# Kernel tuning notes

Hardware: AMD Instinct MI355X
Metric: run time of the kernel (lower is better)

## Reference

```python
import jax, jax.numpy as jnp
import numpy as np

B, N, DIM, H, DH, M = 2, 2048, 1024, 16, 64, 512
INNER = H * DH  # 1024
KV = M + 1 + N  # xl mem + null kv + sequence = 2561


def rotate_half(x):
    x1, x2 = jnp.split(x, 2, axis=-1)
    return jnp.concatenate([-x2, x1], axis=-1)


def apply_rotary_pos_emb(pos, t):
    return t * jnp.cos(pos) + rotate_half(t) * jnp.sin(pos)


def setup_inputs() -> dict:
    key = jax.random.key(0)
    ks = jax.random.split(key, 8)
    return {
        "x": jax.random.normal(ks[0], (B, N, DIM), jnp.float32),
        "rotary_q": jax.random.uniform(ks[1], (N, DH), jnp.float32) * 6.28,
        "rotary_k": jax.random.uniform(ks[2], (KV, DH), jnp.float32) * 6.28,
        "xl_memories": jax.random.normal(ks[3], (2, B, H, M, DH), jnp.float32) * 0.02,
        "Wq": jax.random.normal(ks[4], (DIM, INNER), jnp.float32) * 0.02,
        "Wkv": jax.random.normal(ks[5], (DIM, 2 * INNER), jnp.float32) * 0.02,
        "Wout": jax.random.normal(ks[6], (INNER, INNER), jnp.float32) * 0.02,
        "null_kv": jax.random.normal(ks[7], (2, H, DH), jnp.float32),
    }


def reference(x, rotary_q, rotary_k, xl_memories, Wq, Wkv, Wout, null_kv):
    # QKV projections (no bias, matching keras Dense(use_bias=False))
    q = (x @ Wq).reshape(B, N, H, DH).transpose(0, 2, 1, 3)  # b h n d
    k, v = jnp.split(x @ Wkv, 2, axis=-1)
    k = k.reshape(B, N, H, DH).transpose(0, 2, 1, 3)
    v = v.reshape(B, N, H, DH).transpose(0, 2, 1, 3)

    # prepend learned null key/value (1 token)
    nk = jnp.broadcast_to(null_kv[0][None, :, None, :], (B, H, 1, DH))
    nv = jnp.broadcast_to(null_kv[1][None, :, None, :], (B, H, 1, DH))
    k = jnp.concatenate([nk, k], axis=2)
    v = jnp.concatenate([nv, v], axis=2)

    next_xl_memories = jnp.stack([k, v])  # [2, b, h, 1+n, d]

    # prepend XL memories along key axis
    k = jnp.concatenate([xl_memories[0], k], axis=2)  # b h kv d
    v = jnp.concatenate([xl_memories[1], v], axis=2)

    # inline rotary embedding on q and (full) k
    q = apply_rotary_pos_emb(rotary_q, q)
    k = apply_rotary_pos_emb(rotary_k, k)

    # causal attention with bottom-right aligned mask (mem/null tokens visible)
    scale = DH ** -0.5
    sim = jnp.einsum('bhid,bhjd->bhij', q, k) * scale  # b h n kv
    i = jnp.arange(N)[:, None]
    j = jnp.arange(KV)[None, :]
    causal_ok = j <= (i + (KV - N))
    sim = jnp.where(causal_ok, sim, jnp.finfo(sim.dtype).min)
    attn = jax.nn.softmax(sim, axis=-1)
    out = jnp.einsum('bhij,bhjd->bhid', attn, v)  # b h n d

    out = out.transpose(0, 2, 1, 3).reshape(B, N, INNER)
    return out @ Wout, next_xl_memories
```

## Files before the change

### kernel.cpp

```cpp
#include <hip/hip_runtime.h>
#include <hip/hip_bf16.h>


typedef short v8s __attribute__((ext_vector_type(8)));
typedef float v4f __attribute__((ext_vector_type(4)));

__device__ __forceinline__ float bf2f(unsigned short x) {
  return __uint_as_float(((unsigned)x) << 16);
}
__device__ __forceinline__ unsigned short f2bf(float f) {
  unsigned u = __float_as_uint(f);
  u += 0x7FFFu + ((u >> 16) & 1u);
  return (unsigned short)(u >> 16);
}

#if __has_builtin(__builtin_amdgcn_exp2f)
#define EXP2(x) __builtin_amdgcn_exp2f(x)
#else
#define EXP2(x) exp2f(x)
#endif

__device__ __forceinline__ void gld_lds16(const void* g, void* l) {
  __builtin_amdgcn_global_load_lds(
      (const __attribute__((address_space(1))) unsigned int*)g,
      (__attribute__((address_space(3))) unsigned int*)l, 16, 0, 0);
}

__device__ __forceinline__ unsigned pk_bf16(float lo, float hi) {
  union { __hip_bfloat162 h; unsigned u; } cv;
  cv.h = __float22bfloat162_rn(make_float2(lo, hi));
  return cv.u;
}

__global__ __launch_bounds__(256) void cvt_bf16(
    const float* __restrict__ S, unsigned short* __restrict__ D, int n4)
{
  const int i = blockIdx.x * 256 + threadIdx.x;
  if (i < n4) {
    const float4 v = ((const float4*)S)[i];
    ushort4 o;
    o.x = f2bf(v.x); o.y = f2bf(v.y); o.z = f2bf(v.z); o.w = f2bf(v.w);
    ((ushort4*)D)[i] = o;
  }
}

template <typename CT>
__global__ __launch_bounds__(256, 2) void gemm_bf16(
    const unsigned short* __restrict__ A,
    const unsigned short* __restrict__ WT,
    CT* __restrict__ C,
    int K, int ldc)
{
  __shared__ unsigned short As[128 * 64];
  __shared__ unsigned short Bs[128 * 64];
  const int tid  = threadIdx.x;
  const int wave = tid >> 6, lane = tid & 63;
  const int l15  = lane & 15, quad = lane >> 4;
  const int wm   = wave >> 1, wn = wave & 1;
  const int row0 = blockIdx.x * 128, col0 = blockIdx.y * 128;
  const int lrow = lane >> 3;
  const int gsw  = (lane & 7) ^ lrow;

  v4f acc[4][4];
  const v4f vzero = {0.f, 0.f, 0.f, 0.f};
#pragma unroll
  for (int i = 0; i < 4; ++i)
#pragma unroll
    for (int j = 0; j < 4; ++j) acc[i][j] = vzero;

  for (int k0 = 0; k0 < K; k0 += 64) {
    __syncthreads();
#pragma unroll
    for (int ro = 0; ro < 4; ++ro) {
      const int chunk = wave * 4 + ro;
      const int arow  = chunk * 8 + lrow;
      gld_lds16(A  + (size_t)(row0 + arow) * K + k0 + gsw * 8, As + chunk * 512);
      gld_lds16(WT + (size_t)(col0 + arow) * K + k0 + gsw * 8, Bs + chunk * 512);
    }
    __syncthreads();

    v8s af[4][2], bf[4][2];
#pragma unroll
    for (int tm = 0; tm < 4; ++tm) {
      const int r = wm * 64 + tm * 16 + l15;
#pragma unroll
      for (int kk = 0; kk < 2; ++kk) {
        const int slot = (kk * 4 + quad) ^ (r & 7);
        af[tm][kk] = *(const v8s*)(As + r * 64 + slot * 8);
      }
    }
#pragma unroll
    for (int tn = 0; tn < 4; ++tn) {
      const int r = wn * 64 + tn * 16 + l15;
#pragma unroll
      for (int kk = 0; kk < 2; ++kk) {
        const int slot = (kk * 4 + quad) ^ (r & 7);
        bf[tn][kk] = *(const v8s*)(Bs + r * 64 + slot * 8);
      }
    }
#pragma unroll
    for (int kk = 0; kk < 2; ++kk)
#pragma unroll
      for (int tm = 0; tm < 4; ++tm)
#pragma unroll
        for (int tn = 0; tn < 4; ++tn)
          acc[tm][tn] = __builtin_amdgcn_mfma_f32_16x16x32_bf16(
              af[tm][kk], bf[tn][kk], acc[tm][tn], 0, 0, 0);
  }

#pragma unroll
  for (int tm = 0; tm < 4; ++tm)
#pragma unroll
    for (int tn = 0; tn < 4; ++tn)
#pragma unroll
      for (int r = 0; r < 4; ++r) {
        const int row = row0 + wm * 64 + tm * 16 + quad * 4 + r;
        const int col = col0 + wn * 64 + tn * 16 + l15;
        if constexpr (sizeof(CT) == 2)
          C[(size_t)row * ldc + col] = (CT)f2bf(acc[tm][tn][r]);
        else
          C[(size_t)row * ldc + col] = (CT)acc[tm][tn][r];
      }
}

__global__ __launch_bounds__(256) void transpose_wt(
    const float* __restrict__ S0,
    const float* __restrict__ S1,
    int c0, int c1, int K,
    unsigned short* __restrict__ D)
{
  __shared__ float T[64][65];
  const int k0 = blockIdx.x * 64, n0 = blockIdx.y * 64;
  const int tid = threadIdx.x;
#pragma unroll
  for (int ro = 0; ro < 4; ++ro) {
    const int idx = ro * 256 + tid;
    const int kr = idx >> 4, ch = idx & 15;
    const int n = n0 + ch * 4;
    float4 val;
    if (n < c0) val = *(const float4*)(S0 + (size_t)(k0 + kr) * c0 + n);
    else        val = *(const float4*)(S1 + (size_t)(k0 + kr) * c1 + (n - c0));
    T[kr][ch * 4 + 0] = val.x; T[kr][ch * 4 + 1] = val.y;
    T[kr][ch * 4 + 2] = val.z; T[kr][ch * 4 + 3] = val.w;
  }
  __syncthreads();
#pragma unroll
  for (int ro = 0; ro < 2; ++ro) {
    const int idx = ro * 256 + tid;
    const int nl = idx >> 3, ch = idx & 7;
    __align__(16) unsigned short tmp[8];
#pragma unroll
    for (int e = 0; e < 8; ++e) tmp[e] = f2bf(T[ch * 8 + e][nl]);
    *(uint4*)(D + (size_t)(n0 + nl) * K + k0 + ch * 8) = *(const uint4*)tmp;
  }
}

__global__ __launch_bounds__(256) void assemble(
    const unsigned short* __restrict__ QKV,
    const float* __restrict__ rq,
    const float* __restrict__ rk,
    const float* __restrict__ xlm,
    const float* __restrict__ nkv,
    unsigned short* __restrict__ Qrot,
    unsigned short* __restrict__ Kf,
    unsigned short* __restrict__ Vn,
    float* __restrict__ nxl)
{
  const int gw = blockIdx.x * 4 + (threadIdx.x >> 6);
  const int d  = threadIdx.x & 63;
  const int RK = 32 * 2561;
  const int RQ = 32 * 2048;
  if (gw < RK) {
    const int bh = gw / 2561;
    const int j  = gw - bh * 2561;
    const int b  = bh >> 4, h = bh & 15;
    float kx, vx;
    if (j < 512) {
      const size_t i0 = (((size_t)(b * 16 + h)) * 512 + j) * 64 + d;
      kx = xlm[i0];
      vx = xlm[1048576 + i0];
    } else if (j == 512) {
      kx = nkv[h * 64 + d];
      vx = nkv[1024 + h * 64 + d];
    } else {
      const size_t rowb = ((size_t)(b * 2048 + (j - 513))) * 3072;
      kx = bf2f(QKV[rowb + 1024 + h * 64 + d]);
      vx = bf2f(QKV[rowb + 2048 + h * 64 + d]);
    }
    Vn[(((size_t)bh) * 2561 + j) * 64 + d] = f2bf(vx);
    if (j >= 512) {
      const size_t o0 = (((size_t)(b * 16 + h)) * 2049 + (j - 512)) * 64 + d;
      nxl[o0] = kx;
      nxl[4196352 + o0] = vx;
    }
    const float ang = rk[j * 64 + d];
    const float cs = __cosf(ang), sn = __sinf(ang);
    const float part = __shfl_xor(kx, 32);
    const float kr = kx * cs + (d < 32 ? -part : part) * sn;
    Kf[(((size_t)bh) * 2624 + j) * 64 + d] = f2bf(kr);
  } else if (gw < RK + RQ) {
    const int g2 = gw - RK;
    const int bh = g2 >> 11, n = g2 & 2047;
    const int b  = bh >> 4, h = bh & 15;
    const float qx = bf2f(QKV[((size_t)(b * 2048 + n)) * 3072 + h * 64 + d]);
    const float ang = rq[n * 64 + d];
    const float cs = __cosf(ang), sn = __sinf(ang);
    const float part = __shfl_xor(qx, 32);
    const float qr = qx * cs + (d < 32 ? -part : part) * sn;
    Qrot[(((size_t)bh) * 2048 + n) * 64 + d] = f2bf(qr * 0.18033688f);
  } else {
    const int g3 = gw - RK - RQ;
    const int bh = g3 / 63;
    const int jj = 2561 + (g3 - bh * 63);
    Kf[(((size_t)bh) * 2624 + jj) * 64 + d] = 0;
  }
}

__global__ __launch_bounds__(256) void transpose_v(
    const unsigned short* __restrict__ Vn,
    unsigned short* __restrict__ VTp)
{
  __shared__ unsigned short T[64][72];
  const int j0 = blockIdx.x * 64;
  const int bh = blockIdx.y;
  const int tid = threadIdx.x;
#pragma unroll
  for (int ro = 0; ro < 2; ++ro) {
    const int idx = ro * 256 + tid;
    const int jr = idx >> 3, ch = idx & 7;
    uint4 val = make_uint4(0, 0, 0, 0);
    if (j0 + jr < 2561)
      val = *(const uint4*)(Vn + (((size_t)bh) * 2561 + j0 + jr) * 64 + ch * 8);
    *(uint4*)(&T[jr][ch * 8]) = val;
  }
  __syncthreads();
#pragma unroll
  for (int ro = 0; ro < 2; ++ro) {
    const int idx = ro * 256 + tid;
    const int dl = idx >> 3, ch = idx & 7;
    __align__(16) unsigned short tmp[8];
#pragma unroll
    for (int e = 0; e < 8; ++e) {
      const int kappa = ch * 8 + e;
      const int sig = (kappa & 32) + ((e & 4) << 2) + ((ch & 3) << 2) + (e & 3);
      tmp[e] = T[sig][dl];
    }
    *(uint4*)(VTp + (((size_t)bh) * 64 + dl) * 2624 + j0 + ch * 8) = *(const uint4*)tmp;
  }
}

__global__ __launch_bounds__(256, 4) void attn_fa(
    const unsigned short* __restrict__ Qr,
    const unsigned short* __restrict__ Kf,
    const unsigned short* __restrict__ VTp,
    unsigned short* __restrict__ Ao)
{
  const int bh = blockIdx.y;
  const int qb = 31 - (int)((blockIdx.x + blockIdx.y) & 31);
  const int b = bh >> 4, h = bh & 15;
  __shared__ unsigned short Ks[2][64 * 72];
  __shared__ unsigned short Vs[2][64 * 72];
  const int tid = threadIdx.x;
  const int wave = tid >> 6, lane = tid & 63;
  const int l15 = lane & 15, quad = lane >> 4;
  const v4f vzero = {0.f, 0.f, 0.f, 0.f};

  v8s qf[2];
  {
    const unsigned short* Qg =
        Qr + (((size_t)bh) * 2048 + qb * 64 + wave * 16 + l15) * 64;
    qf[0] = *(const v8s*)(Qg + quad * 8);
    qf[1] = *(const v8s*)(Qg + 32 + quad * 8);
  }
  const int qbase = qb * 64 + wave * 16 + l15 + 513;

  v4f O[4], Ol;
#pragma unroll
  for (int dt = 0; dt < 4; ++dt) O[dt] = vzero;
  Ol = vzero;
  const short one_bf = (short)0x3F80;
  const v8s ones = {one_bf, one_bf, one_bf, one_bf,
                    one_bf, one_bf, one_bf, one_bf};

  const unsigned short* Kg0 = Kf + (size_t)bh * 2624 * 64;
  const unsigned short* Vg0 = VTp + (size_t)bh * 64 * 2624;
  const int ntiles = (qb + 10 <= 41) ? (qb + 10) : 41;
  const int tfast  = qb + 7;

  const int srow = tid >> 3, sch = tid & 7;
  const int srow1 = srow + 32;
  uint4 ka, kb, va, vb;

#define PREFETCH(t)                                                          \
  {                                                                          \
    const int j0p = (t) * 64;                                                \
    ka = *(const uint4*)(Kg0 + (size_t)(j0p + srow) * 64 + sch * 8);         \
    va = *(const uint4*)(Vg0 + (size_t)srow * 2624 + j0p + sch * 8);         \
    kb = *(const uint4*)(Kg0 + (size_t)(j0p + srow1) * 64 + sch * 8);        \
    vb = *(const uint4*)(Vg0 + (size_t)srow1 * 2624 + j0p + sch * 8);        \
  }
#define STAGE(bi)                                                            \
  {                                                                          \
    *(uint4*)(Ks[bi] + srow * 72 + sch * 8) = ka;                            \
    *(uint4*)(Vs[bi] + srow * 72 + sch * 8) = va;                            \
    *(uint4*)(Ks[bi] + srow1 * 72 + sch * 8) = kb;                           \
    *(uint4*)(Vs[bi] + srow1 * 72 + sch * 8) = vb;                           \
  }

  auto compute_tile = [&](const unsigned short* Ksb, const unsigned short* Vsb,
                          int j0, bool masked) {
    v4f s[4];
#pragma unroll
    for (int jt = 0; jt < 4; ++jt) {
      const v8s kfr0 = *(const v8s*)(Ksb + (jt * 16 + l15) * 72 + quad * 8);
      const v8s kfr1 = *(const v8s*)(Ksb + (jt * 16 + l15) * 72 + 32 + quad * 8);
      v4f c = vzero;
      c = __builtin_amdgcn_mfma_f32_16x16x32_bf16(kfr0, qf[0], c, 0, 0, 0);
      c = __builtin_amdgcn_mfma_f32_16x16x32_bf16(kfr1, qf[1], c, 0, 0, 0);
      s[jt] = c;
    }

    if (masked) {
#pragma unroll
      for (int jt = 0; jt < 4; ++jt) {
        const int jrow = j0 + jt * 16 + quad * 4;
#pragma unroll
        for (int r = 0; r < 4; ++r)
          s[jt][r] = (jrow + r <= qbase) ? s[jt][r] : -1e30f;
      }
    }

    union { unsigned u[4]; v8s s8; } pk0, pk1;
    pk0.u[0] = pk_bf16(EXP2(s[0][0]), EXP2(s[0][1]));
    pk0.u[1] = pk_bf16(EXP2(s[0][2]), EXP2(s[0][3]));
    pk0.u[2] = pk_bf16(EXP2(s[1][0]), EXP2(s[1][1]));
    pk0.u[3] = pk_bf16(EXP2(s[1][2]), EXP2(s[1][3]));
    pk1.u[0] = pk_bf16(EXP2(s[2][0]), EXP2(s[2][1]));
    pk1.u[1] = pk_bf16(EXP2(s[2][2]), EXP2(s[2][3]));
    pk1.u[2] = pk_bf16(EXP2(s[3][0]), EXP2(s[3][1]));
    pk1.u[3] = pk_bf16(EXP2(s[3][2]), EXP2(s[3][3]));

#pragma unroll
    for (int dt = 0; dt < 4; ++dt) {
      const v8s vf0 = *(const v8s*)(Vsb + (dt * 16 + l15) * 72 + quad * 8);
      const v8s vf1 = *(const v8s*)(Vsb + (dt * 16 + l15) * 72 + 32 + quad * 8);
      v4f c = O[dt];
      c = __builtin_amdgcn_mfma_f32_16x16x32_bf16(pk0.s8, vf0, c, 0, 0, 0);
      c = __builtin_amdgcn_mfma_f32_16x16x32_bf16(pk1.s8, vf1, c, 0, 0, 0);
      O[dt] = c;
    }
    Ol = __builtin_amdgcn_mfma_f32_16x16x32_bf16(pk0.s8, ones, Ol, 0, 0, 0);
    Ol = __builtin_amdgcn_mfma_f32_16x16x32_bf16(pk1.s8, ones, Ol, 0, 0, 0);
  };

  PREFETCH(0);
  STAGE(0);
  PREFETCH(1);
  __syncthreads();
  for (int t = 0; t < ntiles; ++t) {
    if (t + 1 < ntiles) {
      STAGE((t + 1) & 1);
      if (t + 2 < ntiles) PREFETCH(t + 2);
    }
    compute_tile(Ks[t & 1], Vs[t & 1], t * 64, t > tfast);
    __syncthreads();
  }
#undef PREFETCH
#undef STAGE

#pragma unroll
  for (int r = 0; r < 4; ++r) {
    const float linv = 1.0f / Ol[r];
    const int n = qb * 64 + wave * 16 + quad * 4 + r;
    const size_t rowbase = ((size_t)b * 2048 + n) * 1024 + h * 64;
#pragma unroll
    for (int dt = 0; dt < 4; ++dt)
      Ao[rowbase + dt * 16 + l15] = f2bf(O[dt][r] * linv);
  }
}

extern "C" void kernel_launch(void* const* d_in, const int* in_sizes, int n_in,
                              void* d_out, int out_size, void* d_ws, size_t ws_size,
                              hipStream_t stream)
{
  const float* x    = (const float*)d_in[0];
  const float* rq   = (const float*)d_in[1];
  const float* rk   = (const float*)d_in[2];
  const float* xlm  = (const float*)d_in[3];
  const float* Wq   = (const float*)d_in[4];
  const float* Wkv  = (const float*)d_in[5];
  const float* Wout = (const float*)d_in[6];
  const float* nkv  = (const float*)d_in[7];
  float* out = (float*)d_out;
  float* nxl = out + 4194304;
  char* ws = (char*)d_ws;
  unsigned short* QKV   = (unsigned short*)(ws + 0);
  unsigned short* xbf   = (unsigned short*)(ws + 25165824);
  unsigned short* Ao    = (unsigned short*)(ws + 25165824);
  unsigned short* WqkvT = (unsigned short*)(ws + 33554432);
  unsigned short* WoutT = (unsigned short*)(ws + 39845888);
  unsigned short* Qrot  = (unsigned short*)(ws + 41943040);
  unsigned short* Kf    = (unsigned short*)(ws + 50331648);
  unsigned short* Vn    = (unsigned short*)(ws + 61079552);
  unsigned short* VTp   = (unsigned short*)(ws + 71569408);

  cvt_bf16<<<4096, 256, 0, stream>>>(x, xbf, 1048576);
  transpose_wt<<<dim3(16, 48), 256, 0, stream>>>(Wq, Wkv, 1024, 2048, 1024, WqkvT);
  transpose_wt<<<dim3(16, 16), 256, 0, stream>>>(Wout, Wout, 1024, 1024, 1024, WoutT);
  gemm_bf16<unsigned short><<<dim3(32, 24), 256, 0, stream>>>(xbf, WqkvT, QKV, 1024, 3072);
  assemble<<<37376, 256, 0, stream>>>(QKV, rq, rk, xlm, nkv, Qrot, Kf, Vn, nxl);
  transpose_v<<<dim3(41, 32), 256, 0, stream>>>(Vn, VTp);
  attn_fa<<<dim3(32, 32), 256, 0, stream>>>(Qrot, Kf, VTp, Ao);
  gemm_bf16<float><<<dim3(32, 8), 256, 0, stream>>>(Ao, WoutT, out, 1024, 1024);
}
```

Before: 229.5 us.

## Switch attention to 32x32 MFMA with direct global K/V fragment loads

Rewrites the attention kernel so each 64-thread wave handles 32 query rows using 32x32x16 bf16 MFMA instead of 16x16x32 tiles. The block drops to 128 threads and no longer stages K/V through double-buffered LDS; each lane loads its MFMA fragments straight from global memory. The V transpose permutation and the block-to-work mapping change to match. This removes the LDS staging and barrier cost and raises MFMA work per instruction, but relies on cache hits for the repeated K/V reads and leaves global load latency exposed with no explicit prefetch.

```diff
diff --git a/kernel.cpp b/kernel.cpp
--- a/kernel.cpp
+++ b/kernel.cpp
@@ -4,6 +4,7 @@
 
 typedef short v8s __attribute__((ext_vector_type(8)));
 typedef float v4f __attribute__((ext_vector_type(4)));
+typedef float v16f __attribute__((ext_vector_type(16)));
 
 __device__ __forceinline__ float bf2f(unsigned short x) {
   return __uint_as_float(((unsigned)x) << 16);
@@ -241,141 +242,124 @@
     __align__(16) unsigned short tmp[8];
 #pragma unroll
     for (int e = 0; e < 8; ++e) {
-      const int kappa = ch * 8 + e;
-      const int sig = (kappa & 32) + ((e & 4) << 2) + ((ch & 3) << 2) + (e & 3);
+      const int sig = (e & 3) + ((ch & 3) << 2) + ((e & 4) << 2) + ((ch & 4) << 3);
       tmp[e] = T[sig][dl];
     }
     *(uint4*)(VTp + (((size_t)bh) * 64 + dl) * 2624 + j0 + ch * 8) = *(const uint4*)tmp;
   }
 }
 
-__global__ __launch_bounds__(256, 4) void attn_fa(
+__global__ __launch_bounds__(128, 2) void attn_fa(
     const unsigned short* __restrict__ Qr,
     const unsigned short* __restrict__ Kf,
     const unsigned short* __restrict__ VTp,
     unsigned short* __restrict__ Ao)
 {
-  const int bh = blockIdx.y;
-  const int qb = 31 - (int)((blockIdx.x + blockIdx.y) & 31);
+  const int bh = blockIdx.x;
+  const int qb = 31 - (int)((blockIdx.x * 9 + blockIdx.y) & 31);
   const int b = bh >> 4, h = bh & 15;
-  __shared__ unsigned short Ks[2][64 * 72];
-  __shared__ unsigned short Vs[2][64 * 72];
   const int tid = threadIdx.x;
-  const int wave = tid >> 6, lane = tid & 63;
-  const int l15 = lane & 15, quad = lane >> 4;
-  const v4f vzero = {0.f, 0.f, 0.f, 0.f};
-
-  v8s qf[2];
+  const int w = tid >> 6;
+  const int lane = tid & 63;
+  const int l31 = lane & 31, hf = lane >> 5;
+
+  v8s qf[4];
   {
     const unsigned short* Qg =
-        Qr + (((size_t)bh) * 2048 + qb * 64 + wave * 16 + l15) * 64;
-    qf[0] = *(const v8s*)(Qg + quad * 8);
-    qf[1] = *(const v8s*)(Qg + 32 + quad * 8);
-  }
-  const int qbase = qb * 64 + wave * 16 + l15 + 513;
-
-  v4f O[4], Ol;
-#pragma unroll
-  for (int dt = 0; dt < 4; ++dt) O[dt] = vzero;
-  Ol = vzero;
+        Qr + (((size_t)bh) * 2048 + qb * 64 + w * 32 + l31) * 64 + hf * 8;
+#pragma unroll
+    for (int kb = 0; kb < 4; ++kb) qf[kb] = *(const v8s*)(Qg + kb * 16);
+  }
+  const int qbase = qb * 64 + w * 32 + l31 + 513;
+
+  v16f O0 = {0,0,0,0,0,0,0,0,0,0,0,0,0,0,0,0};
+  v16f O1 = {0,0,0,0,0,0,0,0,0,0,0,0,0,0,0,0};
+  v16f Olv = {0,0,0,0,0,0,0,0,0,0,0,0,0,0,0,0};
   const short one_bf = (short)0x3F80;
   const v8s ones = {one_bf, one_bf, one_bf, one_bf,
                     one_bf, one_bf, one_bf, one_bf};
 
-  const unsigned short* Kg0 = Kf + (size_t)bh * 2624 * 64;
-  const unsigned short* Vg0 = VTp + (size_t)bh * 64 * 2624;
-  const int ntiles = (qb + 10 <= 41) ? (qb + 10) : 41;
+  const unsigned short* Kg =
+      Kf + ((size_t)bh * 2624 + l31) * 64 + hf * 8;
+  const unsigned short* V0 =
+      VTp + ((size_t)bh * 64 + l31) * 2624 + hf * 8;
+  const unsigned short* V1 = V0 + (size_t)32 * 2624;
+
+  const int ntiles = qb + 10;
   const int tfast  = qb + 7;
 
-  const int srow = tid >> 3, sch = tid & 7;
-  const int srow1 = srow + 32;
-  uint4 ka, kb, va, vb;
-
-#define PREFETCH(t)                                                          \
-  {                                                                          \
-    const int j0p = (t) * 64;                                                \
-    ka = *(const uint4*)(Kg0 + (size_t)(j0p + srow) * 64 + sch * 8);         \
-    va = *(const uint4*)(Vg0 + (size_t)srow * 2624 + j0p + sch * 8);         \
-    kb = *(const uint4*)(Kg0 + (size_t)(j0p + srow1) * 64 + sch * 8);        \
-    vb = *(const uint4*)(Vg0 + (size_t)srow1 * 2624 + j0p + sch * 8);        \
-  }
-#define STAGE(bi)                                                            \
-  {                                                                          \
-    *(uint4*)(Ks[bi] + srow * 72 + sch * 8) = ka;                            \
-    *(uint4*)(Vs[bi] + srow * 72 + sch * 8) = va;                            \
-    *(uint4*)(Ks[bi] + srow1 * 72 + sch * 8) = kb;                           \
-    *(uint4*)(Vs[bi] + srow1 * 72 + sch * 8) = vb;                           \
-  }
-
-  auto compute_tile = [&](const unsigned short* Ksb, const unsigned short* Vsb,
-                          int j0, bool masked) {
-    v4f s[4];
-#pragma unroll
-    for (int jt = 0; jt < 4; ++jt) {
-      const v8s kfr0 = *(const v8s*)(Ksb + (jt * 16 + l15) * 72 + quad * 8);
-      const v8s kfr1 = *(const v8s*)(Ksb + (jt * 16 + l15) * 72 + 32 + quad * 8);
-      v4f c = vzero;
-      c = __builtin_amdgcn_mfma_f32_16x16x32_bf16(kfr0, qf[0], c, 0, 0, 0);
-      c = __builtin_amdgcn_mfma_f32_16x16x32_bf16(kfr1, qf[1], c, 0, 0, 0);
-      s[jt] = c;
-    }
-
-    if (masked) {
-#pragma unroll
-      for (int jt = 0; jt < 4; ++jt) {
-        const int jrow = j0 + jt * 16 + quad * 4;
-#pragma unroll
-        for (int r = 0; r < 4; ++r)
-          s[jt][r] = (jrow + r <= qbase) ? s[jt][r] : -1e30f;
-      }
-    }
-
-    union { unsigned u[4]; v8s s8; } pk0, pk1;
-    pk0.u[0] = pk_bf16(EXP2(s[0][0]), EXP2(s[0][1]));
-    pk0.u[1] = pk_bf16(EXP2(s[0][2]), EXP2(s[0][3]));
-    pk0.u[2] = pk_bf16(EXP2(s[1][0]), EXP2(s[1][1]));
-    pk0.u[3] = pk_bf16(EXP2(s[1][2]), EXP2(s[1][3]));
-    pk1.u[0] = pk_bf16(EXP2(s[2][0]), EXP2(s[2][1]));
-    pk1.u[1] = pk_bf16(EXP2(s[2][2]), EXP2(s[2][3]));
-    pk1.u[2] = pk_bf16(EXP2(s[3][0]), EXP2(s[3][1]));
-    pk1.u[3] = pk_bf16(EXP2(s[3][2]), EXP2(s[3][3]));
-
-#pragma unroll
-    for (int dt = 0; dt < 4; ++dt) {
-      const v8s vf0 = *(const v8s*)(Vsb + (dt * 16 + l15) * 72 + quad * 8);
-      const v8s vf1 = *(const v8s*)(Vsb + (dt * 16 + l15) * 72 + 32 + quad * 8);
-      v4f c = O[dt];
-      c = __builtin_amdgcn_mfma_f32_16x16x32_bf16(pk0.s8, vf0, c, 0, 0, 0);
-      c = __builtin_amdgcn_mfma_f32_16x16x32_bf16(pk1.s8, vf1, c, 0, 0, 0);
-      O[dt] = c;
-    }
-    Ol = __builtin_amdgcn_mfma_f32_16x16x32_bf16(pk0.s8, ones, Ol, 0, 0, 0);
-    Ol = __builtin_amdgcn_mfma_f32_16x16x32_bf16(pk1.s8, ones, Ol, 0, 0, 0);
-  };
-
-  PREFETCH(0);
-  STAGE(0);
-  PREFETCH(1);
-  __syncthreads();
   for (int t = 0; t < ntiles; ++t) {
-    if (t + 1 < ntiles) {
-      STAGE((t + 1) & 1);
-      if (t + 2 < ntiles) PREFETCH(t + 2);
-    }
-    compute_tile(Ks[t & 1], Vs[t & 1], t * 64, t > tfast);
-    __syncthreads();
-  }
-#undef PREFETCH
-#undef STAGE
-
-#pragma unroll
-  for (int r = 0; r < 4; ++r) {
-    const float linv = 1.0f / Ol[r];
-    const int n = qb * 64 + wave * 16 + quad * 4 + r;
+    const int j64 = t * 64;
+
+    v8s kf0[4], kf1[4];
+    {
+      const unsigned short* Kl = Kg + (size_t)j64 * 64;
+#pragma unroll
+      for (int kb = 0; kb < 4; ++kb) {
+        kf0[kb] = *(const v8s*)(Kl + kb * 16);
+        kf1[kb] = *(const v8s*)(Kl + 2048 + kb * 16);
+      }
+    }
+
+    v16f s0 = {0,0,0,0,0,0,0,0,0,0,0,0,0,0,0,0};
+    v16f s1 = {0,0,0,0,0,0,0,0,0,0,0,0,0,0,0,0};
+#pragma unroll
+    for (int kb = 0; kb < 4; ++kb) {
+      s0 = __builtin_amdgcn_mfma_f32_32x32x16_bf16(kf0[kb], qf[kb], s0, 0, 0, 0);
+      s1 = __builtin_amdgcn_mfma_f32_32x32x16_bf16(kf1[kb], qf[kb], s1, 0, 0, 0);
+    }
+
+    if (t > tfast) {
+#pragma unroll
+      for (int reg = 0; reg < 16; ++reg) {
+        const int krow = (reg & 3) + 8 * (reg >> 2) + 4 * hf;
+        s0[reg] = (j64 + krow <= qbase) ? s0[reg] : -1e30f;
+        s1[reg] = (j64 + 32 + krow <= qbase) ? s1[reg] : -1e30f;
+      }
+    }
+
+    union PK { unsigned u[4]; v8s s8; };
+    PK pa00, pa01, pa10, pa11;
+    pa00.u[0] = pk_bf16(EXP2(s0[0]),  EXP2(s0[1]));
+    pa00.u[1] = pk_bf16(EXP2(s0[2]),  EXP2(s0[3]));
+    pa00.u[2] = pk_bf16(EXP2(s0[8]),  EXP2(s0[9]));
+    pa00.u[3] = pk_bf16(EXP2(s0[10]), EXP2(s0[11]));
+    pa01.u[0] = pk_bf16(EXP2(s0[4]),  EXP2(s0[5]));
+    pa01.u[1] = pk_bf16(EXP2(s0[6]),  EXP2(s0[7]));
+    pa01.u[2] = pk_bf16(EXP2(s0[12]), EXP2(s0[13]));
+    pa01.u[3] = pk_bf16(EXP2(s0[14]), EXP2(s0[15]));
+    pa10.u[0] = pk_bf16(EXP2(s1[0]),  EXP2(s1[1]));
+    pa10.u[1] = pk_bf16(EXP2(s1[2]),  EXP2(s1[3]));
+    pa10.u[2] = pk_bf16(EXP2(s1[8]),  EXP2(s1[9]));
+    pa10.u[3] = pk_bf16(EXP2(s1[10]), EXP2(s1[11]));
+    pa11.u[0] = pk_bf16(EXP2(s1[4]),  EXP2(s1[5]));
+    pa11.u[1] = pk_bf16(EXP2(s1[6]),  EXP2(s1[7]));
+    pa11.u[2] = pk_bf16(EXP2(s1[12]), EXP2(s1[13]));
+    pa11.u[3] = pk_bf16(EXP2(s1[14]), EXP2(s1[15]));
+
+#define PV_STEP(pa_, kvoff)                                                   \
+    {                                                                         \
+      const v8s vf0 = *(const v8s*)(V0 + j64 + (kvoff));                      \
+      const v8s vf1 = *(const v8s*)(V1 + j64 + (kvoff));                      \
+      O0  = __builtin_amdgcn_mfma_f32_32x32x16_bf16(pa_.s8, vf0,  O0,  0,0,0);\
+      O1  = __builtin_amdgcn_mfma_f32_32x32x16_bf16(pa_.s8, vf1,  O1,  0,0,0);\
+      Olv = __builtin_amdgcn_mfma_f32_32x32x16_bf16(pa_.s8, ones, Olv, 0,0,0);\
+    }
+    PV_STEP(pa00, 0);
+    PV_STEP(pa01, 16);
+    PV_STEP(pa10, 32);
+    PV_STEP(pa11, 48);
+#undef PV_STEP
+  }
+
+#pragma unroll
+  for (int reg = 0; reg < 16; ++reg) {
+    const int qloc = (reg & 3) + 8 * (reg >> 2) + 4 * hf;
+    const float linv = 1.0f / Olv[reg];
+    const int n = qb * 64 + w * 32 + qloc;
     const size_t rowbase = ((size_t)b * 2048 + n) * 1024 + h * 64;
-#pragma unroll
-    for (int dt = 0; dt < 4; ++dt)
-      Ao[rowbase + dt * 16 + l15] = f2bf(O[dt][r] * linv);
+    Ao[rowbase + l31]      = f2bf(O0[reg] * linv);
+    Ao[rowbase + 32 + l31] = f2bf(O1[reg] * linv);
   }
 }
 
@@ -410,6 +394,6 @@
   gemm_bf16<unsigned short><<<dim3(32, 24), 256, 0, stream>>>(xbf, WqkvT, QKV, 1024, 3072);
   assemble<<<37376, 256, 0, stream>>>(QKV, rq, rk, xlm, nkv, Qrot, Kf, Vn, nxl);
   transpose_v<<<dim3(41, 32), 256, 0, stream>>>(Vn, VTp);
-  attn_fa<<<dim3(32, 32), 256, 0, stream>>>(Qrot, Kf, VTp, Ao);
+  attn_fa<<<dim3(32, 32), 128, 0, stream>>>(Qrot, Kf, VTp, Ao);
   gemm_bf16<float><<<dim3(32, 8), 256, 0, stream>>>(Ao, WoutT, out, 1024, 1024);
 }
```

Measured after the change: 298.5 us. +30.0%, slower.

## Give each attention wave two 16-row query tiles and halve block size

Applied to the files above, without the earlier changes.

The flash-attention kernel now runs 2 waves per block instead of 4, with each wave handling 32 query rows as two 16-row MFMA tiles. Each K/V fragment read from LDS is reused across both query tiles, which halves LDS fragment traffic per FLOP. Each thread also stages four rows of K and V instead of two. The cost is higher register pressure (doubled O accumulators and score tiles) and fewer threads per block to hide latency. Launch bounds also change to (128, 2).

```diff
diff --git a/kernel.cpp b/kernel.cpp
--- a/kernel.cpp
+++ b/kernel.cpp
@@ -249,7 +249,7 @@
   }
 }
 
-__global__ __launch_bounds__(256, 4) void attn_fa(
+__global__ __launch_bounds__(128, 2) void attn_fa(
     const unsigned short* __restrict__ Qr,
     const unsigned short* __restrict__ Kf,
     const unsigned short* __restrict__ VTp,
@@ -261,23 +261,28 @@
   __shared__ unsigned short Ks[2][64 * 72];
   __shared__ unsigned short Vs[2][64 * 72];
   const int tid = threadIdx.x;
-  const int wave = tid >> 6, lane = tid & 63;
+  const int wave = tid >> 6;
+  const int lane = tid & 63;
   const int l15 = lane & 15, quad = lane >> 4;
   const v4f vzero = {0.f, 0.f, 0.f, 0.f};
 
-  v8s qf[2];
-  {
+  v8s qf[2][2];
+#pragma unroll
+  for (int mt = 0; mt < 2; ++mt) {
     const unsigned short* Qg =
-        Qr + (((size_t)bh) * 2048 + qb * 64 + wave * 16 + l15) * 64;
-    qf[0] = *(const v8s*)(Qg + quad * 8);
-    qf[1] = *(const v8s*)(Qg + 32 + quad * 8);
-  }
-  const int qbase = qb * 64 + wave * 16 + l15 + 513;
-
-  v4f O[4], Ol;
-#pragma unroll
-  for (int dt = 0; dt < 4; ++dt) O[dt] = vzero;
-  Ol = vzero;
+        Qr + (((size_t)bh) * 2048 + qb * 64 + wave * 32 + mt * 16 + l15) * 64;
+    qf[mt][0] = *(const v8s*)(Qg + quad * 8);
+    qf[mt][1] = *(const v8s*)(Qg + 32 + quad * 8);
+  }
+  const int qb0 = qb * 64 + wave * 32 + l15 + 513;
+
+  v4f O[2][4], Ol[2];
+#pragma unroll
+  for (int mt = 0; mt < 2; ++mt) {
+#pragma unroll
+    for (int dt = 0; dt < 4; ++dt) O[mt][dt] = vzero;
+    Ol[mt] = vzero;
+  }
   const short one_bf = (short)0x3F80;
   const v8s ones = {one_bf, one_bf, one_bf, one_bf,
                     one_bf, one_bf, one_bf, one_bf};
@@ -288,69 +293,89 @@
   const int tfast  = qb + 7;
 
   const int srow = tid >> 3, sch = tid & 7;
-  const int srow1 = srow + 32;
-  uint4 ka, kb, va, vb;
+  uint4 kk[4], vv[4];
 
 #define PREFETCH(t)                                                          \
   {                                                                          \
     const int j0p = (t) * 64;                                                \
-    ka = *(const uint4*)(Kg0 + (size_t)(j0p + srow) * 64 + sch * 8);         \
-    va = *(const uint4*)(Vg0 + (size_t)srow * 2624 + j0p + sch * 8);         \
-    kb = *(const uint4*)(Kg0 + (size_t)(j0p + srow1) * 64 + sch * 8);        \
-    vb = *(const uint4*)(Vg0 + (size_t)srow1 * 2624 + j0p + sch * 8);        \
+    _Pragma("unroll")                                                        \
+    for (int i = 0; i < 4; ++i) {                                            \
+      kk[i] = *(const uint4*)(Kg0 + (size_t)(j0p + srow + 16 * i) * 64 +     \
+                              sch * 8);                                      \
+      vv[i] = *(const uint4*)(Vg0 + (size_t)(srow + 16 * i) * 2624 + j0p +   \
+                              sch * 8);                                      \
+    }                                                                        \
   }
 #define STAGE(bi)                                                            \
   {                                                                          \
-    *(uint4*)(Ks[bi] + srow * 72 + sch * 8) = ka;                            \
-    *(uint4*)(Vs[bi] + srow * 72 + sch * 8) = va;                            \
-    *(uint4*)(Ks[bi] + srow1 * 72 + sch * 8) = kb;                           \
-    *(uint4*)(Vs[bi] + srow1 * 72 + sch * 8) = vb;                           \
+    _Pragma("unroll")                                                        \
+    for (int i = 0; i < 4; ++i) {                                            \
+      *(uint4*)(Ks[bi] + (srow + 16 * i) * 72 + sch * 8) = kk[i];            \
+      *(uint4*)(Vs[bi] + (srow + 16 * i) * 72 + sch * 8) = vv[i];            \
+    }                                                                        \
   }
 
   auto compute_tile = [&](const unsigned short* Ksb, const unsigned short* Vsb,
                           int j0, bool masked) {
-    v4f s[4];
+    v4f s[2][4];
 #pragma unroll
     for (int jt = 0; jt < 4; ++jt) {
       const v8s kfr0 = *(const v8s*)(Ksb + (jt * 16 + l15) * 72 + quad * 8);
       const v8s kfr1 = *(const v8s*)(Ksb + (jt * 16 + l15) * 72 + 32 + quad * 8);
-      v4f c = vzero;
-      c = __builtin_amdgcn_mfma_f32_16x16x32_bf16(kfr0, qf[0], c, 0, 0, 0);
-      c = __builtin_amdgcn_mfma_f32_16x16x32_bf16(kfr1, qf[1], c, 0, 0, 0);
-      s[jt] = c;
+#pragma unroll
+      for (int mt = 0; mt < 2; ++mt) {
+        v4f c = vzero;
+        c = __builtin_amdgcn_mfma_f32_16x16x32_bf16(kfr0, qf[mt][0], c, 0, 0, 0);
+        c = __builtin_amdgcn_mfma_f32_16x16x32_bf16(kfr1, qf[mt][1], c, 0, 0, 0);
+        s[mt][jt] = c;
+      }
     }
 
     if (masked) {
 #pragma unroll
-      for (int jt = 0; jt < 4; ++jt) {
-        const int jrow = j0 + jt * 16 + quad * 4;
-#pragma unroll
-        for (int r = 0; r < 4; ++r)
-          s[jt][r] = (jrow + r <= qbase) ? s[jt][r] : -1e30f;
-      }
-    }
-
-    union { unsigned u[4]; v8s s8; } pk0, pk1;
-    pk0.u[0] = pk_bf16(EXP2(s[0][0]), EXP2(s[0][1]));
-    pk0.u[1] = pk_bf16(EXP2(s[0][2]), EXP2(s[0][3]));
-    pk0.u[2] = pk_bf16(EXP2(s[1][0]), EXP2(s[1][1]));
-    pk0.u[3] = pk_bf16(EXP2(s[1][2]), EXP2(s[1][3]));
-    pk1.u[0] = pk_bf16(EXP2(s[2][0]), EXP2(s[2][1]));
-    pk1.u[1] = pk_bf16(EXP2(s[2][2]), EXP2(s[2][3]));
-    pk1.u[2] = pk_bf16(EXP2(s[3][0]), EXP2(s[3][1]));
-    pk1.u[3] = pk_bf16(EXP2(s[3][2]), EXP2(s[3][3]));
+      for (int mt = 0; mt < 2; ++mt) {
+        const int qbase = qb0 + mt * 16;
+#pragma unroll
+        for (int jt = 0; jt < 4; ++jt) {
+          const int jrow = j0 + jt * 16 + quad * 4;
+#pragma unroll
+          for (int r = 0; r < 4; ++r)
+            s[mt][jt][r] = (jrow + r <= qbase) ? s[mt][jt][r] : -1e30f;
+        }
+      }
+    }
+
+    union PK { unsigned u[4]; v8s s8; };
+    PK pk0[2], pk1[2];
+#pragma unroll
+    for (int mt = 0; mt < 2; ++mt) {
+      pk0[mt].u[0] = pk_bf16(EXP2(s[mt][0][0]), EXP2(s[mt][0][1]));
+      pk0[mt].u[1] = pk_bf16(EXP2(s[mt][0][2]), EXP2(s[mt][0][3]));
+      pk0[mt].u[2] = pk_bf16(EXP2(s[mt][1][0]), EXP2(s[mt][1][1]));
+      pk0[mt].u[3] = pk_bf16(EXP2(s[mt][1][2]), EXP2(s[mt][1][3]));
+      pk1[mt].u[0] = pk_bf16(EXP2(s[mt][2][0]), EXP2(s[mt][2][1]));
+      pk1[mt].u[1] = pk_bf16(EXP2(s[mt][2][2]), EXP2(s[mt][2][3]));
+      pk1[mt].u[2] = pk_bf16(EXP2(s[mt][3][0]), EXP2(s[mt][3][1]));
+      pk1[mt].u[3] = pk_bf16(EXP2(s[mt][3][2]), EXP2(s[mt][3][3]));
+    }
 
 #pragma unroll
     for (int dt = 0; dt < 4; ++dt) {
       const v8s vf0 = *(const v8s*)(Vsb + (dt * 16 + l15) * 72 + quad * 8);
       const v8s vf1 = *(const v8s*)(Vsb + (dt * 16 + l15) * 72 + 32 + quad * 8);
-      v4f c = O[dt];
-      c = __builtin_amdgcn_mfma_f32_16x16x32_bf16(pk0.s8, vf0, c, 0, 0, 0);
-      c = __builtin_amdgcn_mfma_f32_16x16x32_bf16(pk1.s8, vf1, c, 0, 0, 0);
-      O[dt] = c;
-    }
-    Ol = __builtin_amdgcn_mfma_f32_16x16x32_bf16(pk0.s8, ones, Ol, 0, 0, 0);
-    Ol = __builtin_amdgcn_mfma_f32_16x16x32_bf16(pk1.s8, ones, Ol, 0, 0, 0);
+#pragma unroll
+      for (int mt = 0; mt < 2; ++mt) {
+        v4f c = O[mt][dt];
+        c = __builtin_amdgcn_mfma_f32_16x16x32_bf16(pk0[mt].s8, vf0, c, 0, 0, 0);
+        c = __builtin_amdgcn_mfma_f32_16x16x32_bf16(pk1[mt].s8, vf1, c, 0, 0, 0);
+        O[mt][dt] = c;
+      }
+    }
+#pragma unroll
+    for (int mt = 0; mt < 2; ++mt) {
+      Ol[mt] = __builtin_amdgcn_mfma_f32_16x16x32_bf16(pk0[mt].s8, ones, Ol[mt], 0, 0, 0);
+      Ol[mt] = __builtin_amdgcn_mfma_f32_16x16x32_bf16(pk1[mt].s8, ones, Ol[mt], 0, 0, 0);
+    }
   };
 
   PREFETCH(0);
@@ -369,14 +394,16 @@
 #undef STAGE
 
 #pragma unroll
-  for (int r = 0; r < 4; ++r) {
-    const float linv = 1.0f / Ol[r];
-    const int n = qb * 64 + wave * 16 + quad * 4 + r;
-    const size_t rowbase = ((size_t)b * 2048 + n) * 1024 + h * 64;
-#pragma unroll
-    for (int dt = 0; dt < 4; ++dt)
-      Ao[rowbase + dt * 16 + l15] = f2bf(O[dt][r] * linv);
-  }
+  for (int mt = 0; mt < 2; ++mt)
+#pragma unroll
+    for (int r = 0; r < 4; ++r) {
+      const float linv = 1.0f / Ol[mt][r];
+      const int n = qb * 64 + wave * 32 + mt * 16 + quad * 4 + r;
+      const size_t rowbase = ((size_t)b * 2048 + n) * 1024 + h * 64;
+#pragma unroll
+      for (int dt = 0; dt < 4; ++dt)
+        Ao[rowbase + dt * 16 + l15] = f2bf(O[mt][dt][r] * linv);
+    }
 }
 
 extern "C" void kernel_launch(void* const* d_in, const int* in_sizes, int n_in,
@@ -410,6 +437,6 @@
   gemm_bf16<unsigned short><<<dim3(32, 24), 256, 0, stream>>>(xbf, WqkvT, QKV, 1024, 3072);
   assemble<<<37376, 256, 0, stream>>>(QKV, rq, rk, xlm, nkv, Qrot, Kf, Vn, nxl);
   transpose_v<<<dim3(41, 32), 256, 0, stream>>>(Vn, VTp);
-  attn_fa<<<dim3(32, 32), 256, 0, stream>>>(Qrot, Kf, VTp, Ao);
+  attn_fa<<<dim3(32, 32), 128, 0, stream>>>(Qrot, Kf, VTp, Ao);
   gemm_bf16<float><<<dim3(32, 8), 256, 0, stream>>>(Ao, WoutT, out, 1024, 1024);
 }
```

Result: slower. 314.4 us (+37.0%).

## Give each attention wave two query sub-tiles to reuse K/V LDS fragments

Applied to the files above, without the earlier changes.

The attention kernel now runs 2 waves per block instead of 4, and each wave handles 32 query rows as two 16-row MFMA sub-tiles. Each K and V fragment read from LDS is used for two MFMAs, which halves LDS fragment traffic per unit of math. Each thread also stages four K/V rows instead of two. The cost is higher register pressure (twice the accumulators and score registers) and fewer waves per block, so there are fewer waves available to hide latency. The launch bounds change to 128 threads with a minimum of 2 blocks per CU.

```diff
diff --git a/kernel.cpp b/kernel.cpp
--- a/kernel.cpp
+++ b/kernel.cpp
@@ -249,7 +249,7 @@
   }
 }
 
-__global__ __launch_bounds__(256, 4) void attn_fa(
+__global__ __launch_bounds__(128, 2) void attn_fa(
     const unsigned short* __restrict__ Qr,
     const unsigned short* __restrict__ Kf,
     const unsigned short* __restrict__ VTp,
@@ -261,23 +261,26 @@
   __shared__ unsigned short Ks[2][64 * 72];
   __shared__ unsigned short Vs[2][64 * 72];
   const int tid = threadIdx.x;
-  const int wave = tid >> 6, lane = tid & 63;
+  const int wave = tid >> 6;
+  const int lane = tid & 63;
   const int l15 = lane & 15, quad = lane >> 4;
   const v4f vzero = {0.f, 0.f, 0.f, 0.f};
 
-  v8s qf[2];
+  v8s qf00, qf01, qf10, qf11;
   {
-    const unsigned short* Qg =
-        Qr + (((size_t)bh) * 2048 + qb * 64 + wave * 16 + l15) * 64;
-    qf[0] = *(const v8s*)(Qg + quad * 8);
-    qf[1] = *(const v8s*)(Qg + 32 + quad * 8);
-  }
-  const int qbase = qb * 64 + wave * 16 + l15 + 513;
-
-  v4f O[4], Ol;
-#pragma unroll
-  for (int dt = 0; dt < 4; ++dt) O[dt] = vzero;
-  Ol = vzero;
+    const unsigned short* Qg0 =
+        Qr + (((size_t)bh) * 2048 + qb * 64 + wave * 32 + l15) * 64;
+    qf00 = *(const v8s*)(Qg0 + quad * 8);
+    qf01 = *(const v8s*)(Qg0 + 32 + quad * 8);
+    const unsigned short* Qg1 = Qg0 + 16 * 64;
+    qf10 = *(const v8s*)(Qg1 + quad * 8);
+    qf11 = *(const v8s*)(Qg1 + 32 + quad * 8);
+  }
+  const int qb0 = qb * 64 + wave * 32 + l15 + 513;
+
+  v4f O00 = vzero, O01 = vzero, O02 = vzero, O03 = vzero;
+  v4f O10 = vzero, O11 = vzero, O12 = vzero, O13 = vzero;
+  v4f Ol0 = vzero, Ol1 = vzero;
   const short one_bf = (short)0x3F80;
   const v8s ones = {one_bf, one_bf, one_bf, one_bf,
                     one_bf, one_bf, one_bf, one_bf};
@@ -288,69 +291,101 @@
   const int tfast  = qb + 7;
 
   const int srow = tid >> 3, sch = tid & 7;
-  const int srow1 = srow + 32;
-  uint4 ka, kb, va, vb;
+  uint4 kk0, kk1, kk2, kk3, vv0, vv1, vv2, vv3;
 
 #define PREFETCH(t)                                                          \
   {                                                                          \
     const int j0p = (t) * 64;                                                \
-    ka = *(const uint4*)(Kg0 + (size_t)(j0p + srow) * 64 + sch * 8);         \
-    va = *(const uint4*)(Vg0 + (size_t)srow * 2624 + j0p + sch * 8);         \
-    kb = *(const uint4*)(Kg0 + (size_t)(j0p + srow1) * 64 + sch * 8);        \
-    vb = *(const uint4*)(Vg0 + (size_t)srow1 * 2624 + j0p + sch * 8);        \
+    kk0 = *(const uint4*)(Kg0 + (size_t)(j0p + srow)      * 64 + sch * 8);   \
+    kk1 = *(const uint4*)(Kg0 + (size_t)(j0p + srow + 16) * 64 + sch * 8);   \
+    kk2 = *(const uint4*)(Kg0 + (size_t)(j0p + srow + 32) * 64 + sch * 8);   \
+    kk3 = *(const uint4*)(Kg0 + (size_t)(j0p + srow + 48) * 64 + sch * 8);   \
+    vv0 = *(const uint4*)(Vg0 + (size_t)(srow)      * 2624 + j0p + sch * 8); \
+    vv1 = *(const uint4*)(Vg0 + (size_t)(srow + 16) * 2624 + j0p + sch * 8); \
+    vv2 = *(const uint4*)(Vg0 + (size_t)(srow + 32) * 2624 + j0p + sch * 8); \
+    vv3 = *(const uint4*)(Vg0 + (size_t)(srow + 48) * 2624 + j0p + sch * 8); \
   }
 #define STAGE(bi)                                                            \
   {                                                                          \
-    *(uint4*)(Ks[bi] + srow * 72 + sch * 8) = ka;                            \
-    *(uint4*)(Vs[bi] + srow * 72 + sch * 8) = va;                            \
-    *(uint4*)(Ks[bi] + srow1 * 72 + sch * 8) = kb;                           \
-    *(uint4*)(Vs[bi] + srow1 * 72 + sch * 8) = vb;                           \
+    *(uint4*)(Ks[bi] + (srow)      * 72 + sch * 8) = kk0;                    \
+    *(uint4*)(Ks[bi] + (srow + 16) * 72 + sch * 8) = kk1;                    \
+    *(uint4*)(Ks[bi] + (srow + 32) * 72 + sch * 8) = kk2;                    \
+    *(uint4*)(Ks[bi] + (srow + 48) * 72 + sch * 8) = kk3;                    \
+    *(uint4*)(Vs[bi] + (srow)      * 72 + sch * 8) = vv0;                    \
+    *(uint4*)(Vs[bi] + (srow + 16) * 72 + sch * 8) = vv1;                    \
+    *(uint4*)(Vs[bi] + (srow + 32) * 72 + sch * 8) = vv2;                    \
+    *(uint4*)(Vs[bi] + (srow + 48) * 72 + sch * 8) = vv3;                    \
   }
 
   auto compute_tile = [&](const unsigned short* Ksb, const unsigned short* Vsb,
                           int j0, bool masked) {
-    v4f s[4];
+    v4f s[2][4];
 #pragma unroll
     for (int jt = 0; jt < 4; ++jt) {
       const v8s kfr0 = *(const v8s*)(Ksb + (jt * 16 + l15) * 72 + quad * 8);
       const v8s kfr1 = *(const v8s*)(Ksb + (jt * 16 + l15) * 72 + 32 + quad * 8);
-      v4f c = vzero;
-      c = __builtin_amdgcn_mfma_f32_16x16x32_bf16(kfr0, qf[0], c, 0, 0, 0);
-      c = __builtin_amdgcn_mfma_f32_16x16x32_bf16(kfr1, qf[1], c, 0, 0, 0);
-      s[jt] = c;
+      v4f c0 = vzero;
+      c0 = __builtin_amdgcn_mfma_f32_16x16x32_bf16(kfr0, qf00, c0, 0, 0, 0);
+      c0 = __builtin_amdgcn_mfma_f32_16x16x32_bf16(kfr1, qf01, c0, 0, 0, 0);
+      s[0][jt] = c0;
+      v4f c1 = vzero;
+      c1 = __builtin_amdgcn_mfma_f32_16x16x32_bf16(kfr0, qf10, c1, 0, 0, 0);
+      c1 = __builtin_amdgcn_mfma_f32_16x16x32_bf16(kfr1, qf11, c1, 0, 0, 0);
+      s[1][jt] = c1;
     }
 
     if (masked) {
 #pragma unroll
-      for (int jt = 0; jt < 4; ++jt) {
-        const int jrow = j0 + jt * 16 + quad * 4;
-#pragma unroll
-        for (int r = 0; r < 4; ++r)
-          s[jt][r] = (jrow + r <= qbase) ? s[jt][r] : -1e30f;
+      for (int mt = 0; mt < 2; ++mt) {
+        const int qbase = qb0 + mt * 16;
+#pragma unroll
+        for (int jt = 0; jt < 4; ++jt) {
+          const int jrow = j0 + jt * 16 + quad * 4;
+#pragma unroll
+          for (int r = 0; r < 4; ++r)
+            s[mt][jt][r] = (jrow + r <= qbase) ? s[mt][jt][r] : -1e30f;
+        }
       }
     }
 
-    union { unsigned u[4]; v8s s8; } pk0, pk1;
-    pk0.u[0] = pk_bf16(EXP2(s[0][0]), EXP2(s[0][1]));
-    pk0.u[1] = pk_bf16(EXP2(s[0][2]), EXP2(s[0][3]));
-    pk0.u[2] = pk_bf16(EXP2(s[1][0]), EXP2(s[1][1]));
-    pk0.u[3] = pk_bf16(EXP2(s[1][2]), EXP2(s[1][3]));
-    pk1.u[0] = pk_bf16(EXP2(s[2][0]), EXP2(s[2][1]));
-    pk1.u[1] = pk_bf16(EXP2(s[2][2]), EXP2(s[2][3]));
-    pk1.u[2] = pk_bf16(EXP2(s[3][0]), EXP2(s[3][1]));
-    pk1.u[3] = pk_bf16(EXP2(s[3][2]), EXP2(s[3][3]));
+    union PK { unsigned u[4]; v8s s8; };
+    PK p0a, p0b, p1a, p1b;
+    p0a.u[0] = pk_bf16(EXP2(s[0][0][0]), EXP2(s[0][0][1]));
+    p0a.u[1] = pk_bf16(EXP2(s[0][0][2]), EXP2(s[0][0][3]));
+    p0a.u[2] = pk_bf16(EXP2(s[0][1][0]), EXP2(s[0][1][1]));
+    p0a.u[3] = pk_bf16(EXP2(s[0][1][2]), EXP2(s[0][1][3]));
+    p0b.u[0] = pk_bf16(EXP2(s[0][2][0]), EXP2(s[0][2][1]));
+    p0b.u[1] = pk_bf16(EXP2(s[0][2][2]), EXP2(s[0][2][3]));
+    p0b.u[2] = pk_bf16(EXP2(s[0][3][0]), EXP2(s[0][3][1]));
+    p0b.u[3] = pk_bf16(EXP2(s[0][3][2]), EXP2(s[0][3][3]));
+    p1a.u[0] = pk_bf16(EXP2(s[1][0][0]), EXP2(s[1][0][1]));
+    p1a.u[1] = pk_bf16(EXP2(s[1][0][2]), EXP2(s[1][0][3]));
+    p1a.u[2] = pk_bf16(EXP2(s[1][1][0]), EXP2(s[1][1][1]));
+    p1a.u[3] = pk_bf16(EXP2(s[1][1][2]), EXP2(s[1][1][3]));
+    p1b.u[0] = pk_bf16(EXP2(s[1][2][0]), EXP2(s[1][2][1]));
+    p1b.u[1] = pk_bf16(EXP2(s[1][2][2]), EXP2(s[1][2][3]));
+    p1b.u[2] = pk_bf16(EXP2(s[1][3][0]), EXP2(s[1][3][1]));
+    p1b.u[3] = pk_bf16(EXP2(s[1][3][2]), EXP2(s[1][3][3]));
 
 #pragma unroll
     for (int dt = 0; dt < 4; ++dt) {
       const v8s vf0 = *(const v8s*)(Vsb + (dt * 16 + l15) * 72 + quad * 8);
       const v8s vf1 = *(const v8s*)(Vsb + (dt * 16 + l15) * 72 + 32 + quad * 8);
-      v4f c = O[dt];
-      c = __builtin_amdgcn_mfma_f32_16x16x32_bf16(pk0.s8, vf0, c, 0, 0, 0);
-      c = __builtin_amdgcn_mfma_f32_16x16x32_bf16(pk1.s8, vf1, c, 0, 0, 0);
-      O[dt] = c;
-    }
-    Ol = __builtin_amdgcn_mfma_f32_16x16x32_bf16(pk0.s8, ones, Ol, 0, 0, 0);
-    Ol = __builtin_amdgcn_mfma_f32_16x16x32_bf16(pk1.s8, ones, Ol, 0, 0, 0);
+      v4f c0 = (dt == 0) ? O00 : (dt == 1) ? O01 : (dt == 2) ? O02 : O03;
+      c0 = __builtin_amdgcn_mfma_f32_16x16x32_bf16(p0a.s8, vf0, c0, 0, 0, 0);
+      c0 = __builtin_amdgcn_mfma_f32_16x16x32_bf16(p0b.s8, vf1, c0, 0, 0, 0);
+      if (dt == 0) O00 = c0; else if (dt == 1) O01 = c0;
+      else if (dt == 2) O02 = c0; else O03 = c0;
+      v4f c1 = (dt == 0) ? O10 : (dt == 1) ? O11 : (dt == 2) ? O12 : O13;
+      c1 = __builtin_amdgcn_mfma_f32_16x16x32_bf16(p1a.s8, vf0, c1, 0, 0, 0);
+      c1 = __builtin_amdgcn_mfma_f32_16x16x32_bf16(p1b.s8, vf1, c1, 0, 0, 0);
+      if (dt == 0) O10 = c1; else if (dt == 1) O11 = c1;
+      else if (dt == 2) O12 = c1; else O13 = c1;
+    }
+    Ol0 = __builtin_amdgcn_mfma_f32_16x16x32_bf16(p0a.s8, ones, Ol0, 0, 0, 0);
+    Ol0 = __builtin_amdgcn_mfma_f32_16x16x32_bf16(p0b.s8, ones, Ol0, 0, 0, 0);
+    Ol1 = __builtin_amdgcn_mfma_f32_16x16x32_bf16(p1a.s8, ones, Ol1, 0, 0, 0);
+    Ol1 = __builtin_amdgcn_mfma_f32_16x16x32_bf16(p1b.s8, ones, Ol1, 0, 0, 0);
   };
 
   PREFETCH(0);
@@ -370,12 +405,19 @@
 
 #pragma unroll
   for (int r = 0; r < 4; ++r) {
-    const float linv = 1.0f / Ol[r];
-    const int n = qb * 64 + wave * 16 + quad * 4 + r;
-    const size_t rowbase = ((size_t)b * 2048 + n) * 1024 + h * 64;
-#pragma unroll
-    for (int dt = 0; dt < 4; ++dt)
-      Ao[rowbase + dt * 16 + l15] = f2bf(O[dt][r] * linv);
+    const float linv0 = 1.0f / Ol0[r];
+    const int n0 = qb * 64 + wave * 32 + quad * 4 + r;
+    const size_t rb0 = ((size_t)b * 2048 + n0) * 1024 + h * 64;
+    Ao[rb0 + 0 * 16 + l15] = f2bf(O00[r] * linv0);
+    Ao[rb0 + 1 * 16 + l15] = f2bf(O01[r] * linv0);
+    Ao[rb0 + 2 * 16 + l15] = f2bf(O02[r] * linv0);
+    Ao[rb0 + 3 * 16 + l15] = f2bf(O03[r] * linv0);
+    const float linv1 = 1.0f / Ol1[r];
+    const size_t rb1 = rb0 + (size_t)16 * 1024;
+    Ao[rb1 + 0 * 16 + l15] = f2bf(O10[r] * linv1);
+    Ao[rb1 + 1 * 16 + l15] = f2bf(O11[r] * linv1);
+    Ao[rb1 + 2 * 16 + l15] = f2bf(O12[r] * linv1);
+    Ao[rb1 + 3 * 16 + l15] = f2bf(O13[r] * linv1);
   }
 }
 
@@ -410,6 +452,6 @@
   gemm_bf16<unsigned short><<<dim3(32, 24), 256, 0, stream>>>(xbf, WqkvT, QKV, 1024, 3072);
   assemble<<<37376, 256, 0, stream>>>(QKV, rq, rk, xlm, nkv, Qrot, Kf, Vn, nxl);
   transpose_v<<<dim3(41, 32), 256, 0, stream>>>(Vn, VTp);
-  attn_fa<<<dim3(32, 32), 256, 0, stream>>>(Qrot, Kf, VTp, Ao);
+  attn_fa<<<dim3(32, 32), 128, 0, stream>>>(Qrot, Kf, VTp, Ao);
   gemm_bf16<float><<<dim3(32, 8), 256, 0, stream>>>(Ao, WoutT, out, 1024, 1024);
 }
```

New measurement: 241.8 us. +5.4%, slower.
